# Optimization experiments

Measured on AMD Instinct MI355X. Metric: run time of the kernel, lower is better.

## Reference

```python
import jax, jax.numpy as jnp
import numpy as np

N = 1024
H = 128


def setup_inputs() -> dict:
    key = jax.random.key(0)
    k1, k2, k3, k4, k5, k6 = jax.random.split(key, 6)
    s = 1.0 / np.sqrt(H)
    return {
        "node_feats": jax.random.normal(k1, (N, H), dtype=jnp.float32),
        "edge_attr": jax.random.normal(k2, (N * N, H), dtype=jnp.float32),
        "We": jax.random.uniform(k3, (H, H), jnp.float32, -s, s),
        "be": jax.random.uniform(k4, (H,), jnp.float32, -s, s),
        "Wi": jax.random.uniform(k5, (H, H), jnp.float32, -s, s),
        "Wj": jax.random.uniform(k6, (H, H), jnp.float32, -s, s),
    }


def reference(node_feats, edge_attr, We, be, Wi, Wj):
    # f_ij: [N^2, H] linear with bias
    f_ij = edge_attr @ We.T + be
    # f_i, f_j: [N, H] linears without bias
    f_i = node_feats @ Wi.T
    f_j = node_feats @ Wj.T
    # torch.matmul on 1-D vectors -> scalar dot; broadcast into each H-wide row.
    dots = jnp.einsum("ih,jh->ij", f_i, f_j)  # [N, N]
    fi_fj = dots.reshape(-1, 1)                 # [N^2, 1], broadcasts over H
    return jax.nn.relu(f_ij + fi_fj)
```

## Files before the change

### kernel.cpp

```cpp
#include <hip/hip_runtime.h>
#include <hip/hip_bf16.h>
#include <stdint.h>
#include <stddef.h>

typedef __bf16 bf16_t;
typedef __bf16 bf16x8 __attribute__((ext_vector_type(8)));
typedef float  f32x4  __attribute__((ext_vector_type(4)));

#define NN 1024
#define H  128
#define TILES 16384
#define GRID  2048

__global__ void k_cvt_we(const float* __restrict__ src, bf16_t* __restrict__ dst) {
    int i = blockIdx.x * 256 + threadIdx.x;
    if (i < H * H) dst[i] = (bf16_t)src[i];
}

__global__ void k_proj(const float* __restrict__ node,
                       const float* __restrict__ Wi,
                       const float* __restrict__ Wj,
                       bf16_t* __restrict__ fi,
                       bf16_t* __restrict__ fj) {
    __shared__ float nrow[H];
    const int row = blockIdx.x;
    const int t   = threadIdx.x;
    const int h   = t & (H - 1);
    const int sel = t >> 7;
    if (t < H) nrow[t] = node[(size_t)row * H + t];
    __syncthreads();
    const float* w = (sel ? Wj : Wi) + (size_t)h * H;
    float acc = 0.f;
    #pragma unroll
    for (int k4 = 0; k4 < H / 4; ++k4) {
        f32x4 wv = *(const f32x4*)(w + k4 * 4);
        f32x4 nv = *(const f32x4*)(&nrow[k4 * 4]);
        acc += nv[0] * wv[0] + nv[1] * wv[1] + nv[2] * wv[2] + nv[3] * wv[3];
    }
    bf16_t* dst = sel ? fj : fi;
    dst[(size_t)row * H + h] = (bf16_t)acc;
}

__global__ __launch_bounds__(256, 4)
void k_dots(const bf16_t* __restrict__ fi,
            const bf16_t* __restrict__ fj,
            float* __restrict__ dots) {
    const int t    = threadIdx.x;
    const int wave = t >> 6;
    const int lane = t & 63;
    const int l15  = lane & 15;
    const int g    = lane >> 4;

    const int bm    = blockIdx.x >> 3;
    const int bn    = blockIdx.x & 7;
    const int ibase = bm * 128 + wave * 32;
    const int jbase = bn * 128;

    f32x4 acc[2][8];
    #pragma unroll
    for (int mf = 0; mf < 2; ++mf)
        #pragma unroll
        for (int nt = 0; nt < 8; ++nt)
            acc[mf][nt] = (f32x4){0.f, 0.f, 0.f, 0.f};

    const bf16_t* a0 = fi + (size_t)(ibase +  0 + l15) * H + g * 8;
    const bf16_t* a1 = fi + (size_t)(ibase + 16 + l15) * H + g * 8;

    #pragma unroll
    for (int kst = 0; kst < 4; ++kst) {
        bf16x8 af0 = *(const bf16x8*)(a0 + kst * 32);
        bf16x8 af1 = *(const bf16x8*)(a1 + kst * 32);
        #pragma unroll
        for (int nt = 0; nt < 8; ++nt) {
            bf16x8 bf = *(const bf16x8*)(fj + (size_t)(jbase + nt * 16 + l15) * H + kst * 32 + g * 8);
            acc[0][nt] = __builtin_amdgcn_mfma_f32_16x16x32_bf16(af0, bf, acc[0][nt], 0, 0, 0);
            acc[1][nt] = __builtin_amdgcn_mfma_f32_16x16x32_bf16(af1, bf, acc[1][nt], 0, 0, 0);
        }
    }

    #pragma unroll
    for (int mf = 0; mf < 2; ++mf) {
        const int rbase = ibase + mf * 16 + g * 4;
        #pragma unroll
        for (int r = 0; r < 4; ++r) {
            #pragma unroll
            for (int nt = 0; nt < 8; ++nt)
                dots[(size_t)(rbase + r) * NN + jbase + nt * 16 + l15] = acc[mf][nt][r];
        }
    }
}

__device__ __forceinline__ void gl_lds16(const float* g, float* l) {
    __builtin_amdgcn_global_load_lds(
        (const __attribute__((address_space(1))) unsigned int*)g,
        (__attribute__((address_space(3))) unsigned int*)l,
        16, 0, 0);
}

__global__ __launch_bounds__(256)
void k_main(const float* __restrict__ edge,
            const bf16_t* __restrict__ web,
            const float* __restrict__ be,
            const float* __restrict__ dots,
            float* __restrict__ out) {
    __shared__ float lds[2][64][H];
    __shared__ float lbias[H];

    const int t    = threadIdx.x;
    const int wave = t >> 6;
    const int lane = t & 63;
    const int l15  = lane & 15;
    const int g    = lane >> 4;

    if (t < H) lbias[t] = be[t];
    __syncthreads();

    const int tile0 = blockIdx.x;

    {
        const float* src = edge + ((size_t)tile0 * 64 + wave * 16) * H + lane * 4;
        float* dst = &lds[0][wave * 16][0];
        #pragma unroll
        for (int i = 0; i < 8; ++i)
            gl_lds16(src + i * 256, dst + i * 256);
    }

    bf16x8 wfr[8][4];
    {
        const bf16_t* wp = web + (size_t)l15 * H + g * 8;
        #pragma unroll
        for (int nt = 0; nt < 8; ++nt)
            #pragma unroll
            for (int kk = 0; kk < 4; ++kk)
                wfr[nt][kk] = *(const bf16x8*)(wp + (size_t)(nt * 16) * H + kk * 32);
    }

    float dvv[8];
    #pragma unroll
    for (int k = 0; k < 8; ++k)
        dvv[k] = dots[(size_t)(tile0 + k * GRID) * 64 + wave * 16 + l15];

    int cur = 0;
    #pragma unroll 1
    for (int k = 0; k < 8; ++k) {
        const size_t tile = (size_t)tile0 + (size_t)k * GRID;

        asm volatile("s_waitcnt vmcnt(8)" ::: "memory");
        __builtin_amdgcn_sched_barrier(0);

        if (k < 7) {
            const float* src = edge + ((tile + GRID) * 64 + wave * 16) * H + lane * 4;
            float* dst = &lds[cur ^ 1][wave * 16][0];
            #pragma unroll
            for (int i = 0; i < 8; ++i)
                gl_lds16(src + i * 256, dst + i * 256);
        }

        const float dv = dvv[k];
        f32x4 acc[8];
        #pragma unroll
        for (int nt = 0; nt < 8; ++nt) {
            f32x4 bvv = *(const f32x4*)(&lbias[nt * 16 + g * 4]);
            #pragma unroll
            for (int r = 0; r < 4; ++r) acc[nt][r] = bvv[r] + dv;
        }

        const float* lrow = &lds[cur][wave * 16 + l15][g * 8];
        #pragma unroll
        for (int kk = 0; kk < 4; ++kk) {
            f32x4 u0 = *(const f32x4*)(lrow + kk * 32);
            f32x4 u1 = *(const f32x4*)(lrow + kk * 32 + 4);
            bf16x8 bfrag;
            #pragma unroll
            for (int i2 = 0; i2 < 4; ++i2) {
                bfrag[i2]     = (bf16_t)u0[i2];
                bfrag[i2 + 4] = (bf16_t)u1[i2];
            }
            #pragma unroll
            for (int nt = 0; nt < 8; ++nt)
                acc[nt] = __builtin_amdgcn_mfma_f32_16x16x32_bf16(wfr[nt][kk], bfrag, acc[nt], 0, 0, 0);
        }

        float* op = out + (tile * 64 + wave * 16 + l15) * H + g * 4;
        #pragma unroll
        for (int nt = 0; nt < 8; ++nt) {
            f32x4 v;
            #pragma unroll
            for (int r = 0; r < 4; ++r) v[r] = fmaxf(acc[nt][r], 0.f);
            *(f32x4*)(op + nt * 16) = v;
        }

        cur ^= 1;
    }
}

extern "C" void kernel_launch(void* const* d_in, const int* in_sizes, int n_in,
                              void* d_out, int out_size, void* d_ws, size_t ws_size,
                              hipStream_t stream) {
    const float* node = (const float*)d_in[0];
    const float* edge = (const float*)d_in[1];
    const float* We   = (const float*)d_in[2];
    const float* be   = (const float*)d_in[3];
    const float* Wi   = (const float*)d_in[4];
    const float* Wj   = (const float*)d_in[5];
    float* out = (float*)d_out;

    char* w = (char*)d_ws;
    bf16_t* fi_bf = (bf16_t*)w;
    bf16_t* fj_bf = (bf16_t*)(w + (256 << 10));
    float*  dots  = (float*)(w + (512 << 10));
    bf16_t* web   = (bf16_t*)(w + (512 << 10) + (4 << 20));

    k_cvt_we<<<(H * H + 255) / 256, 256, 0, stream>>>(We, web);
    k_proj<<<NN, 256, 0, stream>>>(node, Wi, Wj, fi_bf, fj_bf);
    k_dots<<<64, 256, 0, stream>>>(fi_bf, fj_bf, dots);
    k_main<<<GRID, 256, 0, stream>>>(edge, web, be, dots, out);
}
```

Measured before the change: 244.5 us.

## Use single-wave blocks with triple-buffered, XOR-swizzled LDS staging in main kernel

Restructures k_main from 256-thread blocks (4 waves, 64 rows per tile) into 64-thread single-wave blocks processing 16-row tiles, launched as a grid of 8192. Each wave now has a three-deep LDS ring fed by global_load_lds with two tiles in flight, and the LDS layout is XOR-swizzled to cut bank conflicts on the fragment reads. Bias moves from LDS into registers, which removes the block barrier. The costs are more blocks, more register pressure from the pinned weight fragments, and hand-tuned vmcnt waits that must match the issue pattern exactly.

After: 257.1 us. +5.1%, slower.

```diff
diff --git a/kernel.cpp b/kernel.cpp
--- a/kernel.cpp
+++ b/kernel.cpp
@@ -9,8 +9,7 @@
 
 #define NN 1024
 #define H  128
-#define TILES 16384
-#define GRID  2048
+#define GRID 8192
 
 __global__ void k_cvt_we(const float* __restrict__ src, bf16_t* __restrict__ dst) {
     int i = blockIdx.x * 256 + threadIdx.x;
@@ -97,33 +96,19 @@
         16, 0, 0);
 }
 
-__global__ __launch_bounds__(256)
+__global__ __launch_bounds__(64, 2)
 void k_main(const float* __restrict__ edge,
             const bf16_t* __restrict__ web,
             const float* __restrict__ be,
             const float* __restrict__ dots,
             float* __restrict__ out) {
-    __shared__ float lds[2][64][H];
-    __shared__ float lbias[H];
-
-    const int t    = threadIdx.x;
-    const int wave = t >> 6;
-    const int lane = t & 63;
-    const int l15  = lane & 15;
-    const int g    = lane >> 4;
-
-    if (t < H) lbias[t] = be[t];
-    __syncthreads();
-
-    const int tile0 = blockIdx.x;
-
-    {
-        const float* src = edge + ((size_t)tile0 * 64 + wave * 16) * H + lane * 4;
-        float* dst = &lds[0][wave * 16][0];
-        #pragma unroll
-        for (int i = 0; i < 8; ++i)
-            gl_lds16(src + i * 256, dst + i * 256);
-    }
+    __shared__ __align__(16) float buf[3][16][H];
+
+    const int lane  = threadIdx.x;
+    const int l15   = lane & 15;
+    const int g     = lane >> 4;
+    const int lhalf = lane >> 5;
+    const int b16   = (lane & 31) * 16;
 
     bf16x8 wfr[8][4];
     {
@@ -134,42 +119,63 @@
             for (int kk = 0; kk < 4; ++kk)
                 wfr[nt][kk] = *(const bf16x8*)(wp + (size_t)(nt * 16) * H + kk * 32);
     }
+    f32x4 bvv[8];
+    #pragma unroll
+    for (int nt = 0; nt < 8; ++nt)
+        bvv[nt] = *(const f32x4*)(be + nt * 16 + g * 4);
 
     float dvv[8];
     #pragma unroll
     for (int k = 0; k < 8; ++k)
-        dvv[k] = dots[(size_t)(tile0 + k * GRID) * 64 + wave * 16 + l15];
-
-    int cur = 0;
-    #pragma unroll 1
+        dvv[k] = dots[(size_t)(blockIdx.x + k * GRID) * 16 + l15];
+
+    #pragma unroll
+    for (int nt = 0; nt < 8; ++nt) {
+        #pragma unroll
+        for (int kk = 0; kk < 4; ++kk)
+            asm volatile("" : "+v"(wfr[nt][kk]));
+        asm volatile("" : "+v"(bvv[nt]));
+        asm volatile("" : "+v"(dvv[nt]));
+    }
+
+    #define STAGE(K, BI)                                                         \
+        {                                                                        \
+            const char* tb = (const char*)(edge + (size_t)(blockIdx.x + (K) * GRID) * 16 * H); \
+            _Pragma("unroll")                                                    \
+            for (int i = 0; i < 8; ++i) {                                        \
+                const int r = 2 * i + lhalf;                                     \
+                const int srcoff = r * 512 + (b16 ^ ((r & 7) << 4));             \
+                gl_lds16((const float*)(tb + srcoff), &buf[BI][2 * i][0]);       \
+            }                                                                    \
+        }
+
+    STAGE(0, 0)
+    STAGE(1, 1)
+
+    const int sw = (l15 & 7) << 4;
+
+    #pragma unroll
     for (int k = 0; k < 8; ++k) {
-        const size_t tile = (size_t)tile0 + (size_t)k * GRID;
-
-        asm volatile("s_waitcnt vmcnt(8)" ::: "memory");
+        if (k == 0)                 asm volatile("s_waitcnt vmcnt(8)"  ::: "memory");
+        else if (k == 1 || k == 7)  asm volatile("s_waitcnt vmcnt(16)" ::: "memory");
+        else                        asm volatile("s_waitcnt vmcnt(24)" ::: "memory");
         __builtin_amdgcn_sched_barrier(0);
 
-        if (k < 7) {
-            const float* src = edge + ((tile + GRID) * 64 + wave * 16) * H + lane * 4;
-            float* dst = &lds[cur ^ 1][wave * 16][0];
-            #pragma unroll
-            for (int i = 0; i < 8; ++i)
-                gl_lds16(src + i * 256, dst + i * 256);
-        }
+        if (k < 6) STAGE(k + 2, (k + 2) % 3)
 
         const float dv = dvv[k];
         f32x4 acc[8];
         #pragma unroll
         for (int nt = 0; nt < 8; ++nt) {
-            f32x4 bvv = *(const f32x4*)(&lbias[nt * 16 + g * 4]);
-            #pragma unroll
-            for (int r = 0; r < 4; ++r) acc[nt][r] = bvv[r] + dv;
-        }
-
-        const float* lrow = &lds[cur][wave * 16 + l15][g * 8];
+            #pragma unroll
+            for (int r = 0; r < 4; ++r) acc[nt][r] = bvv[nt][r] + dv;
+        }
+
+        const char* lrow = (const char*)&buf[k % 3][0][0] + l15 * 512;
         #pragma unroll
         for (int kk = 0; kk < 4; ++kk) {
-            f32x4 u0 = *(const f32x4*)(lrow + kk * 32);
-            f32x4 u1 = *(const f32x4*)(lrow + kk * 32 + 4);
+            f32x4 u0 = *(const f32x4*)(lrow + kk * 128 + ((g * 32 +  0) ^ sw));
+            f32x4 u1 = *(const f32x4*)(lrow + kk * 128 + ((g * 32 + 16) ^ sw));
             bf16x8 bfrag;
             #pragma unroll
             for (int i2 = 0; i2 < 4; ++i2) {
@@ -181,7 +187,7 @@
                 acc[nt] = __builtin_amdgcn_mfma_f32_16x16x32_bf16(wfr[nt][kk], bfrag, acc[nt], 0, 0, 0);
         }
 
-        float* op = out + (tile * 64 + wave * 16 + l15) * H + g * 4;
+        float* op = out + ((size_t)(blockIdx.x + k * GRID) * 16 + l15) * H + g * 4;
         #pragma unroll
         for (int nt = 0; nt < 8; ++nt) {
             f32x4 v;
@@ -189,9 +195,8 @@
             for (int r = 0; r < 4; ++r) v[r] = fmaxf(acc[nt][r], 0.f);
             *(f32x4*)(op + nt * 16) = v;
         }
-
-        cur ^= 1;
-    }
+    }
+    #undef STAGE
 }
 
 extern "C" void kernel_launch(void* const* d_in, const int* in_sizes, int n_in,
@@ -214,5 +219,5 @@
     k_cvt_we<<<(H * H + 255) / 256, 256, 0, stream>>>(We, web);
     k_proj<<<NN, 256, 0, stream>>>(node, Wi, Wj, fi_bf, fj_bf);
     k_dots<<<64, 256, 0, stream>>>(fi_bf, fj_bf, dots);
-    k_main<<<GRID, 256, 0, stream>>>(edge, web, be, dots, out);
-}
+    k_main<<<GRID, 64, 0, stream>>>(edge, web, be, dots, out);
+}
```
